# Optimization experiments

Measured on AMD Instinct MI355X. Metric: run time of the kernel, lower is better.

The kernel has to match this reference:

```python
import jax, jax.numpy as jnp
import numpy as np
from jax import lax

BN_EPS = 1e-5
# shifts generated by _generate_shifts(8): dy outer loop, dx inner, skipping (0,0);
# circular_shift rolls shifts=(dx, dy) over dims (2, 3) i.e. dx->H axis, dy->W axis
SHIFTS = [(-1, -1), (0, -1), (1, -1), (-1, 0), (1, 0), (-1, 1), (0, 1), (1, 1)]


def setup_inputs() -> dict:
    key = jax.random.key(0)
    k1, k2 = jax.random.split(key)
    x = jax.random.normal(k1, (32, 128, 56, 56), dtype=jnp.float32)
    # 8 paths, each a 3x3 conv [O, I, kh, kw]
    W = jax.random.normal(k2, (8, 128, 128, 3, 3), dtype=jnp.float32) * 0.05
    gamma = jnp.ones((128,), dtype=jnp.float32)
    beta = jnp.zeros((128,), dtype=jnp.float32)
    return {"x": x, "W": W, "gamma": gamma, "beta": beta}


def _conv3x3(x, w):
    return lax.conv_general_dilated(
        x, w, window_strides=(1, 1), padding=((1, 1), (1, 1)),
        dimension_numbers=("NCHW", "OIHW", "NCHW"))


def reference(x, W, gamma, beta):
    # sum of 8 shifted-input 3x3 convs (accumulated, no stack materialized)
    out = _conv3x3(jnp.roll(x, SHIFTS[0], axis=(2, 3)), W[0])
    for i in range(1, len(SHIFTS)):
        out = out + _conv3x3(jnp.roll(x, SHIFTS[i], axis=(2, 3)), W[i])
    # BatchNorm2d, training-mode batch stats (biased variance), eps=1e-5
    mean = jnp.mean(out, axis=(0, 2, 3), keepdims=True)
    var = jnp.mean(jnp.square(out - mean), axis=(0, 2, 3), keepdims=True)
    out = (out - mean) * lax.rsqrt(var + BN_EPS)
    out = out * gamma.reshape(1, -1, 1, 1) + beta.reshape(1, -1, 1, 1)
    return out
```

## Files before the change

### kernel.cpp

```cpp
#include <hip/hip_runtime.h>
#include <hip/hip_bf16.h>


typedef __attribute__((ext_vector_type(8)))  short s16x8;
typedef __attribute__((ext_vector_type(16))) float f32x16;

__device__ __forceinline__ void gload16(const void* g, void* l) {
    __builtin_amdgcn_global_load_lds(
        (const __attribute__((address_space(1))) unsigned int*)g,
        (__attribute__((address_space(3))) unsigned int*)l, 16, 0, 0);
}

__device__ __forceinline__ unsigned short f2bf(float f) {
    __hip_bfloat16 h = __float2bfloat16(f);
    return *(unsigned short*)&h;
}

__global__ __launch_bounds__(256) void transpose_kernel(
    const float* __restrict__ x, unsigned short* __restrict__ xb,
    float* __restrict__ xcols) {
    __shared__ float xt[128][57];
    const int h = blockIdx.x, n = blockIdx.y, t = threadIdx.x;
    for (int it = 0; it < 28; ++it) {
        int idx = it * 256 + t;
        int c = idx / 56, w = idx % 56;
        xt[c][w] = x[(((size_t)n * 128 + c) * 56 + h) * 56 + w];
    }
    __syncthreads();
    for (int it = 0; it < 4; ++it) {
        int unit = it * 256 + t;
        if (unit < 896) {
            int w = unit >> 4, cu = unit & 15;
            unsigned short pk[8];
#pragma unroll
            for (int j = 0; j < 8; ++j) pk[j] = f2bf(xt[cu * 8 + j][w]);
            *(uint4*)(xb + ((((size_t)n * 56 + h) * 56 + w) * 128 + cu * 8)) = *(uint4*)pk;
        }
    }
    for (int it = 0; it < 2; ++it) {
        int idx = it * 256 + t;
        int c = idx & 127, w4 = idx >> 7;
        const int wmap[4] = {54, 55, 0, 1};
        xcols[(((size_t)n * 4 + w4) * 56 + h) * 128 + c] = xt[c][wmap[w4]];
    }
}

__global__ __launch_bounds__(256) void vpack_kernel(
    const float* __restrict__ W, unsigned short* __restrict__ Ap) {
    int idx = blockIdx.x * 256 + threadIdx.x;
    int tap = idx % 25, oc = idx / 25, c = oc % 128, o = oc / 128;
    int a = tap / 5, b = tap % 5;
    const int dxs[8] = {-1, 0, 1, -1, 1, -1, 0, 1};
    const int dys[8] = {-1, -1, -1, 0, 0, 1, 1, 1};
    float s = 0.f;
#pragma unroll
    for (int i = 0; i < 8; ++i) {
        int kh = a - 1 + dxs[i];
        int kw = b - 1 + dys[i];
        if (kh >= 0 && kh < 3 && kw >= 0 && kw < 3)
            s += W[(((size_t)i * 128 + o) * 128 + c) * 9 + kh * 3 + kw];
    }
    int chunk = c >> 4, k = c & 15, ku = k >> 3, j = k & 7, mo = o >> 5;
    size_t off = ((((size_t)chunk * 25 + tap) * 4 + mo) * 64 + (ku * 32 + (o & 31))) * 8 + j;
    Ap[off] = f2bf(s);
}

__global__ __launch_bounds__(256) void ubuild_kernel(
    const float* __restrict__ W, float* __restrict__ U) {
    int idx = blockIdx.x * 256 + threadIdx.x;
    int c = idx % 128, o = (idx / 128) % 128, e = idx / 16384;
    const int dxs[8] = {-1, 0, 1, -1, 1, -1, 0, 1};
    const int dys[8] = {-1, -1, -1, 0, 0, 1, 1, 1};
    float u[15];
#pragma unroll
    for (int k = 0; k < 15; ++k) u[k] = 0.f;
#pragma unroll
    for (int i = 0; i < 8; ++i) {
        if (e < 2) {
            int kh = (e == 0) ? 0 : 2;
            int hh = (e == 0) ? -1 : 56;
            int sr = (hh - dxs[i] + 56) % 56;
            int r = (e == 0) ? (sr == 54 ? 0 : sr == 55 ? 1 : 2)
                             : (sr == 55 ? 0 : sr == 0 ? 1 : 2);
#pragma unroll
            for (int kw = 0; kw < 3; ++kw) {
                int be = kw - 1 - dys[i] + 2;
                u[r * 5 + be] += W[(((size_t)i * 128 + o) * 128 + c) * 9 + kh * 3 + kw];
            }
        } else {
            int kw = (e == 2) ? 0 : 2;
            int ww = (e == 2) ? -1 : 56;
            int sc = (ww - dys[i] + 56) % 56;
            int r = (e == 2) ? (sc == 54 ? 0 : sc == 55 ? 1 : 2)
                             : (sc == 55 ? 0 : sc == 0 ? 1 : 2);
#pragma unroll
            for (int kh = 0; kh < 3; ++kh) {
                int al = kh - 1 - dxs[i] + 2;
                u[r * 5 + al] += W[(((size_t)i * 128 + o) * 128 + c) * 9 + kh * 3 + kw];
            }
        }
    }
#pragma unroll
    for (int k = 0; k < 15; ++k)
        U[(((size_t)e * 15 + k) * 128 + c) * 128 + o] = u[k];
}

__global__ __launch_bounds__(256) void ucbuild_kernel(
    const float* __restrict__ W, float* __restrict__ Uc) {
    int idx = blockIdx.x * 256 + threadIdx.x;
    int c = idx % 128, o = (idx / 128) % 128, cr = idx / 16384;
    int hC = (cr >> 1) ? 55 : 0, wC = (cr & 1) ? 55 : 0;
    int khb = hC ? 2 : 0, kwb = wC ? 2 : 0;
    const int dxs[8] = {-1, 0, 1, -1, 1, -1, 0, 1};
    const int dys[8] = {-1, -1, -1, 0, 0, 1, 1, 1};
    float v[9];
#pragma unroll
    for (int p = 0; p < 9; ++p) v[p] = 0.f;
#pragma unroll
    for (int i = 0; i < 8; ++i)
        v[(dxs[i] + 1) * 3 + (dys[i] + 1)] = W[(((size_t)i * 128 + o) * 128 + c) * 9 + khb * 3 + kwb];
#pragma unroll
    for (int p = 0; p < 9; ++p)
        Uc[(((size_t)cr * 9 + p) * 128 + c) * 128 + o] = v[p];
}

__global__ __launch_bounds__(512, 2) void conv_mfma(
    const unsigned short* __restrict__ xb, const unsigned short* __restrict__ Ap,
    float* __restrict__ out, float* __restrict__ P) {
    __shared__ __align__(16) unsigned short lds[69632];
    unsigned short* xs = lds;
    unsigned short* As = lds + 16384;
    const int tile = blockIdx.x, n = blockIdx.y;
    const int p0 = tile * 512;
    const int t = threadIdx.x, wv = t >> 6, lane = t & 63;
    const int og = wv >> 2, pg = wv & 3;
    const int hstart = p0 / 56 - 2;

    int vB[4];
    bool fval[4];
#pragma unroll
    for (int nn = 0; nn < 4; ++nn) {
        int px = p0 + pg * 128 + nn * 32 + (lane & 31);
        fval[nn] = px < 3136;
        if (px > 3135) px = 3135;
        int h = px / 56, w = px % 56;
        vB[nn] = (lane >> 5) * 16384 + ((h - hstart - 2) * 60 + w) * 16;
    }
    f32x16 acc[2][4];
#pragma unroll
    for (int mm = 0; mm < 2; ++mm)
#pragma unroll
        for (int nn = 0; nn < 4; ++nn)
#pragma unroll
            for (int r = 0; r < 16; ++r) acc[mm][nn][r] = 0.f;

    const unsigned short* xbn = xb + (size_t)n * 401408;

#pragma unroll 1
    for (int ch = 0; ch < 8; ++ch) {
#pragma unroll
        for (int it = 0; it < 4; ++it) {
            int unit = it * 512 + t;
            int u = unit >> 10, ph = unit & 1023;
            if (ph > 899) ph = 899;
            int r = ph / 60, wc2 = ph % 60;
            int gh = ((hstart + r) % 56 + 56) % 56;
            int gw = wc2 - 2;
            gw += (gw < 0) ? 56 : 0;
            gw -= (gw >= 56) ? 56 : 0;
            gload16(xbn + (gh * 56 + gw) * 128 + ch * 16 + u * 8,
                    (char*)xs + (size_t)(it * 512 + wv * 64) * 16);
        }
        const unsigned short* apc = Ap + (size_t)ch * 51200;
#pragma unroll
        for (int it = 0; it < 13; ++it) {
            int unit = it * 512 + t;
            gload16(apc + (size_t)unit * 8,
                    (char*)As + (size_t)(it * 512 + wv * 64) * 16);
        }
        __syncthreads();

#pragma unroll
        for (int tap = 0; tap < 25; ++tap) {
            const int toff = ((tap / 5) * 60 + (tap % 5)) * 16;
            s16x8 a0 = *(const s16x8*)((const char*)As + (size_t)(tap * 4 + og * 2 + 0) * 1024 + lane * 16);
            s16x8 a1 = *(const s16x8*)((const char*)As + (size_t)(tap * 4 + og * 2 + 1) * 1024 + lane * 16);
            s16x8 b0 = *(const s16x8*)((const char*)xs + vB[0] + toff);
            s16x8 b1 = *(const s16x8*)((const char*)xs + vB[1] + toff);
            s16x8 b2 = *(const s16x8*)((const char*)xs + vB[2] + toff);
            s16x8 b3 = *(const s16x8*)((const char*)xs + vB[3] + toff);
            acc[0][0] = __builtin_amdgcn_mfma_f32_32x32x16_bf16(a0, b0, acc[0][0], 0, 0, 0);
            acc[1][0] = __builtin_amdgcn_mfma_f32_32x32x16_bf16(a1, b0, acc[1][0], 0, 0, 0);
            acc[0][1] = __builtin_amdgcn_mfma_f32_32x32x16_bf16(a0, b1, acc[0][1], 0, 0, 0);
            acc[1][1] = __builtin_amdgcn_mfma_f32_32x32x16_bf16(a1, b1, acc[1][1], 0, 0, 0);
            acc[0][2] = __builtin_amdgcn_mfma_f32_32x32x16_bf16(a0, b2, acc[0][2], 0, 0, 0);
            acc[1][2] = __builtin_amdgcn_mfma_f32_32x32x16_bf16(a1, b2, acc[1][2], 0, 0, 0);
            acc[0][3] = __builtin_amdgcn_mfma_f32_32x32x16_bf16(a0, b3, acc[0][3], 0, 0, 0);
            acc[1][3] = __builtin_amdgcn_mfma_f32_32x32x16_bf16(a1, b3, acc[1][3], 0, 0, 0);
        }
        __syncthreads();
    }

    const int slot = (n * 7 + tile) * 4 + pg;
#pragma unroll
    for (int mm = 0; mm < 2; ++mm) {
#pragma unroll
        for (int r = 0; r < 16; ++r) {
            int o = og * 64 + mm * 32 + (r & 3) + ((lane >> 5) << 2) + ((r >> 2) << 3);
            float s = 0.f, q = 0.f;
#pragma unroll
            for (int nn = 0; nn < 4; ++nn) {
                if (fval[nn]) {
                    float v = acc[mm][nn][r];
                    size_t oi = ((size_t)(n * 128 + o)) * 3136 + (p0 + pg * 128 + nn * 32 + (lane & 31));
                    out[oi] = v;
                    s += v;
                    q = fmaf(v, v, q);
                }
            }
#pragma unroll
            for (int off = 1; off < 32; off <<= 1) {
                s += __shfl_xor(s, off);
                q += __shfl_xor(q, off);
            }
            if ((lane & 31) == 0) {
                P[((size_t)slot * 2 + 0) * 128 + o] = s;
                P[((size_t)slot * 2 + 1) * 128 + o] = q;
            }
        }
    }
}

__global__ __launch_bounds__(512) void border_kernel(
    const float* __restrict__ x, const float* __restrict__ xcols,
    const float* __restrict__ U,
    float* __restrict__ corrRow, float* __restrict__ corrCol) {
    __shared__ float xsb[3][128][33];
    __shared__ float red[2][2][64][15];
    const int e = blockIdx.x, n = blockIdx.y, part = blockIdx.z;
    const int t = threadIdx.x, lane = t & 63, wv = t >> 6;
    const int oh = wv & 1, qh = (wv >> 1) & 1, chalf = wv >> 2;
    int rows[3];
    if (e == 0 || e == 2) { rows[0] = 54; rows[1] = 55; rows[2] = 0; }
    else                  { rows[0] = 55; rows[1] = 0;  rows[2] = 1; }
    if (e < 2) {
        for (int it = 0; it < 24; ++it) {
            int idx = it * 512 + t;
            int m = idx & 31, c = (idx >> 5) & 127, r = idx >> 12;
            int g = part * 28 + m - 2;
            g += (g < 0) ? 56 : 0;
            g -= (g >= 56) ? 56 : 0;
            xsb[r][c][m] = x[(((size_t)n * 128 + c) * 56 + rows[r]) * 56 + g];
        }
    } else {
        int w4[3];
#pragma unroll
        for (int r = 0; r < 3; ++r)
            w4[r] = (rows[r] == 54) ? 0 : (rows[r] == 55) ? 1 : (rows[r] == 0) ? 2 : 3;
        for (int it = 0; it < 24; ++it) {
            int idx = it * 512 + t;
            int c = idx & 127, m = (idx >> 7) & 31, r = idx >> 12;
            int g = part * 28 + m - 2;
            g += (g < 0) ? 56 : 0;
            g -= (g >= 56) ? 56 : 0;
            xsb[r][c][m] = xcols[(((size_t)n * 4 + w4[r]) * 56 + g) * 128 + c];
        }
    }
    __syncthreads();
    const int o = oh * 64 + lane;
    const int pxl = qh * 14;
    float corr[14];
#pragma unroll
    for (int k = 0; k < 14; ++k) corr[k] = 0.f;
#pragma unroll 2
    for (int ci = 0; ci < 64; ++ci) {
        const int c = chalf * 64 + ci;
#pragma unroll
        for (int r = 0; r < 3; ++r) {
            float xl[18];
#pragma unroll
            for (int j = 0; j < 18; ++j) xl[j] = xsb[r][c][pxl + j];
#pragma unroll
            for (int be = 0; be < 5; ++be) {
                float u = U[(((size_t)e * 15 + r * 5 + be) * 128 + c) * 128 + o];
#pragma unroll
                for (int k = 0; k < 14; ++k) corr[k] = fmaf(u, xl[k + be], corr[k]);
            }
        }
    }
    if (chalf == 1) {
#pragma unroll
        for (int k = 0; k < 14; ++k) red[qh][oh][lane][k] = corr[k];
    }
    __syncthreads();
    if (chalf == 0) {
#pragma unroll
        for (int k = 0; k < 14; ++k) corr[k] += red[qh][oh][lane][k];
        const int pbase = part * 28 + qh * 14;
        float* dst = (e < 2 ? corrRow + (((size_t)e * 32 + n) * 128 + o) * 56
                            : corrCol + (((size_t)(e - 2) * 32 + n) * 128 + o) * 56) + pbase;
#pragma unroll
        for (int k = 0; k < 14; ++k) dst[k] = corr[k];
    }
}

__global__ __launch_bounds__(256) void corner_kernel(
    const float* __restrict__ xcols, const float* __restrict__ Uc,
    float* __restrict__ cadd) {
    __shared__ float xc[9][128];
    __shared__ float red[2][128];
    const int cr = blockIdx.x, n = blockIdx.y, t = threadIdx.x;
    const int hC = (cr >> 1) ? 55 : 0, wC = (cr & 1) ? 55 : 0;
    const int khb = hC ? 2 : 0, kwb = wC ? 2 : 0;
    for (int it = 0; it < 5; ++it) {
        int idx = it * 256 + t;
        if (idx < 1152) {
            int c = idx & 127, p = idx >> 7;
            int di = p / 3, dj = p % 3;
            int hs = (hC + khb - 1 - (di - 1) + 56) % 56;
            int ws = (wC + kwb - 1 - (dj - 1) + 56) % 56;
            int w4 = (ws == 54) ? 0 : (ws == 55) ? 1 : (ws == 0) ? 2 : 3;
            xc[p][c] = xcols[(((size_t)n * 4 + w4) * 56 + hs) * 128 + c];
        }
    }
    __syncthreads();
    const int o = t & 127, half = t >> 7;
    float corr = 0.f;
    const float* ucb = Uc + ((size_t)cr * 9 * 128) * 128 + o;
#pragma unroll 4
    for (int pc = half * 576; pc < half * 576 + 576; ++pc) {
        int p = pc >> 7, c = pc & 127;
        corr = fmaf(ucb[(size_t)pc * 128], xc[p][c], corr);
    }
    red[half][o] = corr;
    __syncthreads();
    if (t < 128)
        cadd[(size_t)cr * 4096 + n * 128 + t] = red[0][t] + red[1][t];
}

__global__ __launch_bounds__(256) void finalize_kernel(
    const float* __restrict__ P, const float* __restrict__ out,
    const float* __restrict__ corrRow, const float* __restrict__ corrCol,
    const float* __restrict__ cadd,
    const float* __restrict__ gamma, const float* __restrict__ beta,
    float* __restrict__ SS) {
    const int c = blockIdx.x, t = threadIdx.x;
    float s = 0.f, q = 0.f;
    for (int sl = t; sl < 896; sl += 256) {
        s += P[((size_t)sl * 2 + 0) * 128 + c];
        q += P[((size_t)sl * 2 + 1) * 128 + c];
    }
    for (int item = t; item < 7040; item += 256) {
        int n = item / 220, bidx = item % 220;
        int h, w;
        if (bidx < 56)       { h = 0;  w = bidx; }
        else if (bidx < 112) { h = 55; w = bidx - 56; }
        else if (bidx < 166) { w = 0;  h = bidx - 111; }
        else                 { w = 55; h = bidx - 165; }
        float d = 0.f;
        if (h == 0)  d -= corrRow[(((size_t)0 * 32 + n) * 128 + c) * 56 + w];
        if (h == 55) d -= corrRow[(((size_t)1 * 32 + n) * 128 + c) * 56 + w];
        if (w == 0)  d -= corrCol[(((size_t)0 * 32 + n) * 128 + c) * 56 + h];
        if (w == 55) d -= corrCol[(((size_t)1 * 32 + n) * 128 + c) * 56 + h];
        if ((h == 0 || h == 55) && (w == 0 || w == 55)) {
            int cr = (h ? 2 : 0) + (w ? 1 : 0);
            d += cadd[(size_t)cr * 4096 + n * 128 + c];
        }
        float old = out[((size_t)(n * 128 + c)) * 3136 + h * 56 + w];
        s += d;
        q += d * d + 2.f * old * d;
    }
    __shared__ float rs[256], rq[256];
    rs[t] = s; rq[t] = q;
    __syncthreads();
    for (int st = 128; st > 0; st >>= 1) {
        if (t < st) { rs[t] += rs[t + st]; rq[t] += rq[t + st]; }
        __syncthreads();
    }
    if (t == 0) {
        const float inv = 1.f / 100352.f;
        float mean = rs[0] * inv;
        float var  = rq[0] * inv - mean * mean;
        float sc = gamma[c] * rsqrtf(var + 1e-5f);
        SS[c] = sc;
        SS[128 + c] = beta[c] - mean * sc;
    }
}

__global__ __launch_bounds__(256) void bn_apply_kernel(
    float* __restrict__ out, const float* __restrict__ SS,
    const float* __restrict__ corrRow, const float* __restrict__ corrCol,
    const float* __restrict__ cadd) {
    size_t idx = (size_t)blockIdx.x * 256 + threadIdx.x;
    int plane = (int)(idx / 784);
    int rem = (int)(idx % 784);
    int h = rem / 14, w4 = (rem % 14) * 4;
    int c = plane & 127, n = plane >> 7;
    float sc = SS[c], sh = SS[128 + c];
    float4 v = ((float4*)out)[idx];
    float d0 = 0.f, d1 = 0.f, d2 = 0.f, d3 = 0.f;
    if (h == 0 || h == 55) {
        int eh = (h == 55) ? 1 : 0;
        const float4 cr4 = *(const float4*)(corrRow + (((size_t)eh * 32 + n) * 128 + c) * 56 + w4);
        d0 -= cr4.x; d1 -= cr4.y; d2 -= cr4.z; d3 -= cr4.w;
    }
    if (w4 == 0)  d0 -= corrCol[(((size_t)0 * 32 + n) * 128 + c) * 56 + h];
    if (w4 == 52) d3 -= corrCol[(((size_t)1 * 32 + n) * 128 + c) * 56 + h];
    if (h == 0 || h == 55) {
        int hb = (h == 55) ? 2 : 0;
        if (w4 == 0)  d0 += cadd[(size_t)(hb + 0) * 4096 + n * 128 + c];
        if (w4 == 52) d3 += cadd[(size_t)(hb + 1) * 4096 + n * 128 + c];
    }
    v.x = fmaf(v.x + d0, sc, sh);
    v.y = fmaf(v.y + d1, sc, sh);
    v.z = fmaf(v.z + d2, sc, sh);
    v.w = fmaf(v.w + d3, sc, sh);
    ((float4*)out)[idx] = v;
}

extern "C" void kernel_launch(void* const* d_in, const int* in_sizes, int n_in,
                              void* d_out, int out_size, void* d_ws, size_t ws_size,
                              hipStream_t stream) {
    const float* x     = (const float*)d_in[0];
    const float* W     = (const float*)d_in[1];
    const float* gamma = (const float*)d_in[2];
    const float* beta  = (const float*)d_in[3];
    float* out = (float*)d_out;

    char* ws = (char*)d_ws;
    unsigned short* xb = (unsigned short*)ws;
    unsigned short* Ap = (unsigned short*)(ws + 25690112);
    float* U       = (float*)(ws + 26513408);
    float* Uc      = (float*)(ws + 30445568);
    float* P       = (float*)(ws + 32804864);
    float* SS      = (float*)(ws + 34017280);
    float* xcols   = (float*)(ws + 34018304);
    float* corrRow = (float*)(ws + 37688320);
    float* corrCol = (float*)(ws + 39523328);
    float* cadd    = (float*)(ws + 41358336);

    transpose_kernel<<<dim3(56, 32), 256, 0, stream>>>(x, xb, xcols);
    vpack_kernel<<<1600, 256, 0, stream>>>(W, Ap);
    ubuild_kernel<<<256, 256, 0, stream>>>(W, U);
    ucbuild_kernel<<<256, 256, 0, stream>>>(W, Uc);
    conv_mfma<<<dim3(7, 32), 512, 0, stream>>>(xb, Ap, out, P);
    border_kernel<<<dim3(4, 32, 2), 512, 0, stream>>>(x, xcols, U, corrRow, corrCol);
    corner_kernel<<<dim3(4, 32), 256, 0, stream>>>(xcols, Uc, cadd);
    finalize_kernel<<<128, 256, 0, stream>>>(P, out, corrRow, corrCol, cadd, gamma, beta, SS);
    bn_apply_kernel<<<12544, 256, 0, stream>>>(out, SS, corrRow, corrCol, cadd);
}
```

Before: 324.1 us.

## Restructure conv MFMA kernel into 4-wave blocks with double-buffered LDS pipeline

The conv kernel now runs 256 threads per block, with each wave computing all 128 output channels for its pixel group (a 4x4 accumulator tile) instead of splitting channels across two wave groups. Input and weight tiles are double-buffered in LDS and prefetched with explicit vmcnt waits and raw barriers, so the next tap-row's weights and the next channel chunk's input load while MFMAs run. This aims to hide global-load latency and raise MFMA reuse per LDS read. The cost is a doubled accumulator register footprint and fewer waves per CU. The circular-wrap modulo is also replaced with conditional adds.

```diff
diff --git a/kernel.cpp b/kernel.cpp
--- a/kernel.cpp
+++ b/kernel.cpp
@@ -124,16 +124,14 @@
         Uc[(((size_t)cr * 9 + p) * 128 + c) * 128 + o] = v[p];
 }
 
-__global__ __launch_bounds__(512, 2) void conv_mfma(
+__global__ __launch_bounds__(256, 1) void conv_mfma(
     const unsigned short* __restrict__ xb, const unsigned short* __restrict__ Ap,
     float* __restrict__ out, float* __restrict__ P) {
-    __shared__ __align__(16) unsigned short lds[69632];
-    unsigned short* xs = lds;
-    unsigned short* As = lds + 16384;
+    __shared__ __align__(16) unsigned short lds[53248];
     const int tile = blockIdx.x, n = blockIdx.y;
     const int p0 = tile * 512;
     const int t = threadIdx.x, wv = t >> 6, lane = t & 63;
-    const int og = wv >> 2, pg = wv & 3;
+    const int pg = wv;
     const int hstart = p0 / 56 - 2;
 
     int vB[4];
@@ -146,9 +144,9 @@
         int h = px / 56, w = px % 56;
         vB[nn] = (lane >> 5) * 16384 + ((h - hstart - 2) * 60 + w) * 16;
     }
-    f32x16 acc[2][4];
-#pragma unroll
-    for (int mm = 0; mm < 2; ++mm)
+    f32x16 acc[4][4];
+#pragma unroll
+    for (int mm = 0; mm < 4; ++mm)
 #pragma unroll
         for (int nn = 0; nn < 4; ++nn)
 #pragma unroll
@@ -156,57 +154,100 @@
 
     const unsigned short* xbn = xb + (size_t)n * 401408;
 
-#pragma unroll 1
-    for (int ch = 0; ch < 8; ++ch) {
-#pragma unroll
-        for (int it = 0; it < 4; ++it) {
-            int unit = it * 512 + t;
+    auto stage_xs = [&](int ch, int buf) {
+#pragma unroll
+        for (int it = 0; it < 8; ++it) {
+            int unit = it * 256 + t;
             int u = unit >> 10, ph = unit & 1023;
             if (ph > 899) ph = 899;
             int r = ph / 60, wc2 = ph % 60;
-            int gh = ((hstart + r) % 56 + 56) % 56;
+            int gh = hstart + r;
+            gh += (gh < 0) ? 56 : 0;
+            gh -= (gh >= 56) ? 56 : 0;
             int gw = wc2 - 2;
             gw += (gw < 0) ? 56 : 0;
             gw -= (gw >= 56) ? 56 : 0;
             gload16(xbn + (gh * 56 + gw) * 128 + ch * 16 + u * 8,
-                    (char*)xs + (size_t)(it * 512 + wv * 64) * 16);
-        }
-        const unsigned short* apc = Ap + (size_t)ch * 51200;
-#pragma unroll
-        for (int it = 0; it < 13; ++it) {
-            int unit = it * 512 + t;
-            gload16(apc + (size_t)unit * 8,
-                    (char*)As + (size_t)(it * 512 + wv * 64) * 16);
-        }
-        __syncthreads();
-
-#pragma unroll
-        for (int tap = 0; tap < 25; ++tap) {
-            const int toff = ((tap / 5) * 60 + (tap % 5)) * 16;
-            s16x8 a0 = *(const s16x8*)((const char*)As + (size_t)(tap * 4 + og * 2 + 0) * 1024 + lane * 16);
-            s16x8 a1 = *(const s16x8*)((const char*)As + (size_t)(tap * 4 + og * 2 + 1) * 1024 + lane * 16);
-            s16x8 b0 = *(const s16x8*)((const char*)xs + vB[0] + toff);
-            s16x8 b1 = *(const s16x8*)((const char*)xs + vB[1] + toff);
-            s16x8 b2 = *(const s16x8*)((const char*)xs + vB[2] + toff);
-            s16x8 b3 = *(const s16x8*)((const char*)xs + vB[3] + toff);
-            acc[0][0] = __builtin_amdgcn_mfma_f32_32x32x16_bf16(a0, b0, acc[0][0], 0, 0, 0);
-            acc[1][0] = __builtin_amdgcn_mfma_f32_32x32x16_bf16(a1, b0, acc[1][0], 0, 0, 0);
-            acc[0][1] = __builtin_amdgcn_mfma_f32_32x32x16_bf16(a0, b1, acc[0][1], 0, 0, 0);
-            acc[1][1] = __builtin_amdgcn_mfma_f32_32x32x16_bf16(a1, b1, acc[1][1], 0, 0, 0);
-            acc[0][2] = __builtin_amdgcn_mfma_f32_32x32x16_bf16(a0, b2, acc[0][2], 0, 0, 0);
-            acc[1][2] = __builtin_amdgcn_mfma_f32_32x32x16_bf16(a1, b2, acc[1][2], 0, 0, 0);
-            acc[0][3] = __builtin_amdgcn_mfma_f32_32x32x16_bf16(a0, b3, acc[0][3], 0, 0, 0);
-            acc[1][3] = __builtin_amdgcn_mfma_f32_32x32x16_bf16(a1, b3, acc[1][3], 0, 0, 0);
-        }
-        __syncthreads();
+                    (char*)lds + buf * 32768 + (size_t)(it * 256 + wv * 64) * 16);
+        }
+    };
+    auto stage_A = [&](int ch, int tg, int buf) {
+        const unsigned short* src = Ap + (size_t)ch * 51200 + tg * 10240;
+#pragma unroll
+        for (int it = 0; it < 5; ++it) {
+            int unit = it * 256 + t;
+            gload16(src + (size_t)unit * 8,
+                    (char*)lds + 65536 + buf * 20480 + (size_t)(it * 256 + wv * 64) * 16);
+        }
+    };
+
+    stage_xs(0, 0);
+    stage_A(0, 0, 0);
+    asm volatile("s_waitcnt vmcnt(0)" ::: "memory");
+    __builtin_amdgcn_s_barrier();
+    asm volatile("" ::: "memory");
+
+    int abuf = 0;
+#pragma unroll 1
+    for (int ch = 0; ch < 8; ++ch) {
+#pragma unroll 1
+        for (int tg = 0; tg < 5; ++tg) {
+            const bool last = (ch == 7 && tg == 4);
+            if (!last) {
+                int nch = (tg == 4) ? ch + 1 : ch;
+                int ntg = (tg == 4) ? 0 : tg + 1;
+                stage_A(nch, ntg, abuf ^ 1);
+            }
+            bool xsIss = false;
+            if (tg == 0 && ch < 7) { stage_xs(ch + 1, (ch + 1) & 1); xsIss = true; }
+            if (last)       asm volatile("s_waitcnt vmcnt(0)"  ::: "memory");
+            else if (xsIss) asm volatile("s_waitcnt vmcnt(13)" ::: "memory");
+            else            asm volatile("s_waitcnt vmcnt(5)"  ::: "memory");
+            __builtin_amdgcn_s_barrier();
+            asm volatile("" ::: "memory");
+
+            const char* xsBase = (const char*)lds + (ch & 1) * 32768;
+            const char* aBase  = (const char*)lds + 65536 + abuf * 20480;
+            const int rowoff = tg * 960;
+#pragma unroll
+            for (int tl = 0; tl < 5; ++tl) {
+                const int toff = rowoff + tl * 16;
+                s16x8 a0 = *(const s16x8*)(aBase + (size_t)(tl * 4 + 0) * 1024 + lane * 16);
+                s16x8 a1 = *(const s16x8*)(aBase + (size_t)(tl * 4 + 1) * 1024 + lane * 16);
+                s16x8 a2 = *(const s16x8*)(aBase + (size_t)(tl * 4 + 2) * 1024 + lane * 16);
+                s16x8 a3 = *(const s16x8*)(aBase + (size_t)(tl * 4 + 3) * 1024 + lane * 16);
+                s16x8 b0 = *(const s16x8*)(xsBase + vB[0] + toff);
+                s16x8 b1 = *(const s16x8*)(xsBase + vB[1] + toff);
+                s16x8 b2 = *(const s16x8*)(xsBase + vB[2] + toff);
+                s16x8 b3 = *(const s16x8*)(xsBase + vB[3] + toff);
+                acc[0][0] = __builtin_amdgcn_mfma_f32_32x32x16_bf16(a0, b0, acc[0][0], 0, 0, 0);
+                acc[0][1] = __builtin_amdgcn_mfma_f32_32x32x16_bf16(a0, b1, acc[0][1], 0, 0, 0);
+                acc[0][2] = __builtin_amdgcn_mfma_f32_32x32x16_bf16(a0, b2, acc[0][2], 0, 0, 0);
+                acc[0][3] = __builtin_amdgcn_mfma_f32_32x32x16_bf16(a0, b3, acc[0][3], 0, 0, 0);
+                acc[1][0] = __builtin_amdgcn_mfma_f32_32x32x16_bf16(a1, b0, acc[1][0], 0, 0, 0);
+                acc[1][1] = __builtin_amdgcn_mfma_f32_32x32x16_bf16(a1, b1, acc[1][1], 0, 0, 0);
+                acc[1][2] = __builtin_amdgcn_mfma_f32_32x32x16_bf16(a1, b2, acc[1][2], 0, 0, 0);
+                acc[1][3] = __builtin_amdgcn_mfma_f32_32x32x16_bf16(a1, b3, acc[1][3], 0, 0, 0);
+                acc[2][0] = __builtin_amdgcn_mfma_f32_32x32x16_bf16(a2, b0, acc[2][0], 0, 0, 0);
+                acc[2][1] = __builtin_amdgcn_mfma_f32_32x32x16_bf16(a2, b1, acc[2][1], 0, 0, 0);
+                acc[2][2] = __builtin_amdgcn_mfma_f32_32x32x16_bf16(a2, b2, acc[2][2], 0, 0, 0);
+                acc[2][3] = __builtin_amdgcn_mfma_f32_32x32x16_bf16(a2, b3, acc[2][3], 0, 0, 0);
+                acc[3][0] = __builtin_amdgcn_mfma_f32_32x32x16_bf16(a3, b0, acc[3][0], 0, 0, 0);
+                acc[3][1] = __builtin_amdgcn_mfma_f32_32x32x16_bf16(a3, b1, acc[3][1], 0, 0, 0);
+                acc[3][2] = __builtin_amdgcn_mfma_f32_32x32x16_bf16(a3, b2, acc[3][2], 0, 0, 0);
+                acc[3][3] = __builtin_amdgcn_mfma_f32_32x32x16_bf16(a3, b3, acc[3][3], 0, 0, 0);
+            }
+            __builtin_amdgcn_s_barrier();
+            abuf ^= 1;
+        }
     }
 
     const int slot = (n * 7 + tile) * 4 + pg;
 #pragma unroll
-    for (int mm = 0; mm < 2; ++mm) {
+    for (int mm = 0; mm < 4; ++mm) {
 #pragma unroll
         for (int r = 0; r < 16; ++r) {
-            int o = og * 64 + mm * 32 + (r & 3) + ((lane >> 5) << 2) + ((r >> 2) << 3);
+            int o = mm * 32 + (r & 3) + ((lane >> 5) << 2) + ((r >> 2) << 3);
             float s = 0.f, q = 0.f;
 #pragma unroll
             for (int nn = 0; nn < 4; ++nn) {
@@ -443,7 +484,7 @@
     vpack_kernel<<<1600, 256, 0, stream>>>(W, Ap);
     ubuild_kernel<<<256, 256, 0, stream>>>(W, U);
     ucbuild_kernel<<<256, 256, 0, stream>>>(W, Uc);
-    conv_mfma<<<dim3(7, 32), 512, 0, stream>>>(xb, Ap, out, P);
+    conv_mfma<<<dim3(7, 32), 256, 0, stream>>>(xb, Ap, out, P);
     border_kernel<<<dim3(4, 32, 2), 512, 0, stream>>>(x, xcols, U, corrRow, corrCol);
     corner_kernel<<<dim3(4, 32), 256, 0, stream>>>(xcols, Uc, cadd);
     finalize_kernel<<<128, 256, 0, stream>>>(P, out, corrRow, corrCol, cadd, gamma, beta, SS);
```

After: 336.3 us. +3.8%, slower.

## Double-buffer conv input tiles, read weights from global, merge weight-prep kernels

Applied to the files above, without the earlier changes.

The conv kernel now double-buffers the input halo tile in LDS, so the next channel chunk is prefetched while the current one is computed. The weight fragments are read straight from global memory (through the caches) instead of being staged in LDS, which shrinks LDS use and changes launch bounds to one block per CU. The three weight-preparation kernels are merged into a single launch to cut launch overhead, and the row wrap uses conditional adds instead of a modulo. The risks are higher latency on the per-tap global weight loads and less latency hiding at the lower occupancy.

```diff
diff --git a/kernel.cpp b/kernel.cpp
--- a/kernel.cpp
+++ b/kernel.cpp
@@ -45,91 +45,83 @@
     }
 }
 
-__global__ __launch_bounds__(256) void vpack_kernel(
-    const float* __restrict__ W, unsigned short* __restrict__ Ap) {
-    int idx = blockIdx.x * 256 + threadIdx.x;
-    int tap = idx % 25, oc = idx / 25, c = oc % 128, o = oc / 128;
-    int a = tap / 5, b = tap % 5;
+__global__ __launch_bounds__(256) void wprep_kernel(
+    const float* __restrict__ W, unsigned short* __restrict__ Ap,
+    float* __restrict__ U, float* __restrict__ Uc) {
+    const int bx = blockIdx.x, t = threadIdx.x;
     const int dxs[8] = {-1, 0, 1, -1, 1, -1, 0, 1};
     const int dys[8] = {-1, -1, -1, 0, 0, 1, 1, 1};
-    float s = 0.f;
-#pragma unroll
-    for (int i = 0; i < 8; ++i) {
-        int kh = a - 1 + dxs[i];
-        int kw = b - 1 + dys[i];
-        if (kh >= 0 && kh < 3 && kw >= 0 && kw < 3)
-            s += W[(((size_t)i * 128 + o) * 128 + c) * 9 + kh * 3 + kw];
-    }
-    int chunk = c >> 4, k = c & 15, ku = k >> 3, j = k & 7, mo = o >> 5;
-    size_t off = ((((size_t)chunk * 25 + tap) * 4 + mo) * 64 + (ku * 32 + (o & 31))) * 8 + j;
-    Ap[off] = f2bf(s);
-}
-
-__global__ __launch_bounds__(256) void ubuild_kernel(
-    const float* __restrict__ W, float* __restrict__ U) {
-    int idx = blockIdx.x * 256 + threadIdx.x;
-    int c = idx % 128, o = (idx / 128) % 128, e = idx / 16384;
-    const int dxs[8] = {-1, 0, 1, -1, 1, -1, 0, 1};
-    const int dys[8] = {-1, -1, -1, 0, 0, 1, 1, 1};
-    float u[15];
-#pragma unroll
-    for (int k = 0; k < 15; ++k) u[k] = 0.f;
-#pragma unroll
-    for (int i = 0; i < 8; ++i) {
-        if (e < 2) {
-            int kh = (e == 0) ? 0 : 2;
-            int hh = (e == 0) ? -1 : 56;
-            int sr = (hh - dxs[i] + 56) % 56;
-            int r = (e == 0) ? (sr == 54 ? 0 : sr == 55 ? 1 : 2)
-                             : (sr == 55 ? 0 : sr == 0 ? 1 : 2);
-#pragma unroll
-            for (int kw = 0; kw < 3; ++kw) {
-                int be = kw - 1 - dys[i] + 2;
-                u[r * 5 + be] += W[(((size_t)i * 128 + o) * 128 + c) * 9 + kh * 3 + kw];
+    if (bx < 1600) {
+        int idx = bx * 256 + t;
+        int tap = idx % 25, oc = idx / 25, c = oc % 128, o = oc / 128;
+        int a = tap / 5, b = tap % 5;
+        float s = 0.f;
+#pragma unroll
+        for (int i = 0; i < 8; ++i) {
+            int kh = a - 1 + dxs[i];
+            int kw = b - 1 + dys[i];
+            if (kh >= 0 && kh < 3 && kw >= 0 && kw < 3)
+                s += W[(((size_t)i * 128 + o) * 128 + c) * 9 + kh * 3 + kw];
+        }
+        int chunk = c >> 4, k = c & 15, ku = k >> 3, j = k & 7, mo = o >> 5;
+        size_t off = ((((size_t)chunk * 25 + tap) * 4 + mo) * 64 + (ku * 32 + (o & 31))) * 8 + j;
+        Ap[off] = f2bf(s);
+    } else if (bx < 1856) {
+        int idx = (bx - 1600) * 256 + t;
+        int c = idx % 128, o = (idx / 128) % 128, e = idx / 16384;
+        float u[15];
+#pragma unroll
+        for (int k = 0; k < 15; ++k) u[k] = 0.f;
+#pragma unroll
+        for (int i = 0; i < 8; ++i) {
+            if (e < 2) {
+                int kh = (e == 0) ? 0 : 2;
+                int hh = (e == 0) ? -1 : 56;
+                int sr = (hh - dxs[i] + 56) % 56;
+                int r = (e == 0) ? (sr == 54 ? 0 : sr == 55 ? 1 : 2)
+                                 : (sr == 55 ? 0 : sr == 0 ? 1 : 2);
+#pragma unroll
+                for (int kw = 0; kw < 3; ++kw) {
+                    int be = kw - 1 - dys[i] + 2;
+                    u[r * 5 + be] += W[(((size_t)i * 128 + o) * 128 + c) * 9 + kh * 3 + kw];
+                }
+            } else {
+                int kw = (e == 2) ? 0 : 2;
+                int ww = (e == 2) ? -1 : 56;
+                int sc = (ww - dys[i] + 56) % 56;
+                int r = (e == 2) ? (sc == 54 ? 0 : sc == 55 ? 1 : 2)
+                                 : (sc == 55 ? 0 : sc == 0 ? 1 : 2);
+#pragma unroll
+                for (int kh = 0; kh < 3; ++kh) {
+                    int al = kh - 1 - dxs[i] + 2;
+                    u[r * 5 + al] += W[(((size_t)i * 128 + o) * 128 + c) * 9 + kh * 3 + kw];
+                }
             }
-        } else {
-            int kw = (e == 2) ? 0 : 2;
-            int ww = (e == 2) ? -1 : 56;
-            int sc = (ww - dys[i] + 56) % 56;
-            int r = (e == 2) ? (sc == 54 ? 0 : sc == 55 ? 1 : 2)
-                             : (sc == 55 ? 0 : sc == 0 ? 1 : 2);
-#pragma unroll
-            for (int kh = 0; kh < 3; ++kh) {
-                int al = kh - 1 - dxs[i] + 2;
-                u[r * 5 + al] += W[(((size_t)i * 128 + o) * 128 + c) * 9 + kh * 3 + kw];
-            }
-        }
-    }
-#pragma unroll
-    for (int k = 0; k < 15; ++k)
-        U[(((size_t)e * 15 + k) * 128 + c) * 128 + o] = u[k];
-}
-
-__global__ __launch_bounds__(256) void ucbuild_kernel(
-    const float* __restrict__ W, float* __restrict__ Uc) {
-    int idx = blockIdx.x * 256 + threadIdx.x;
-    int c = idx % 128, o = (idx / 128) % 128, cr = idx / 16384;
-    int hC = (cr >> 1) ? 55 : 0, wC = (cr & 1) ? 55 : 0;
-    int khb = hC ? 2 : 0, kwb = wC ? 2 : 0;
-    const int dxs[8] = {-1, 0, 1, -1, 1, -1, 0, 1};
-    const int dys[8] = {-1, -1, -1, 0, 0, 1, 1, 1};
-    float v[9];
-#pragma unroll
-    for (int p = 0; p < 9; ++p) v[p] = 0.f;
-#pragma unroll
-    for (int i = 0; i < 8; ++i)
-        v[(dxs[i] + 1) * 3 + (dys[i] + 1)] = W[(((size_t)i * 128 + o) * 128 + c) * 9 + khb * 3 + kwb];
-#pragma unroll
-    for (int p = 0; p < 9; ++p)
-        Uc[(((size_t)cr * 9 + p) * 128 + c) * 128 + o] = v[p];
-}
-
-__global__ __launch_bounds__(512, 2) void conv_mfma(
+        }
+#pragma unroll
+        for (int k = 0; k < 15; ++k)
+            U[(((size_t)e * 15 + k) * 128 + c) * 128 + o] = u[k];
+    } else {
+        int idx = (bx - 1856) * 256 + t;
+        int c = idx % 128, o = (idx / 128) % 128, cr = idx / 16384;
+        int hC = (cr >> 1) ? 55 : 0, wC = (cr & 1) ? 55 : 0;
+        int khb = hC ? 2 : 0, kwb = wC ? 2 : 0;
+        float v[9];
+#pragma unroll
+        for (int p = 0; p < 9; ++p) v[p] = 0.f;
+#pragma unroll
+        for (int i = 0; i < 8; ++i)
+            v[(dxs[i] + 1) * 3 + (dys[i] + 1)] = W[(((size_t)i * 128 + o) * 128 + c) * 9 + khb * 3 + kwb];
+#pragma unroll
+        for (int p = 0; p < 9; ++p)
+            Uc[(((size_t)cr * 9 + p) * 128 + c) * 128 + o] = v[p];
+    }
+}
+
+__global__ __launch_bounds__(512, 1) void conv_mfma(
     const unsigned short* __restrict__ xb, const unsigned short* __restrict__ Ap,
     float* __restrict__ out, float* __restrict__ P) {
-    __shared__ __align__(16) unsigned short lds[69632];
-    unsigned short* xs = lds;
-    unsigned short* As = lds + 16384;
+    __shared__ __align__(16) unsigned short lds[32768];
     const int tile = blockIdx.x, n = blockIdx.y;
     const int p0 = tile * 512;
     const int t = threadIdx.x, wv = t >> 6, lane = t & 63;
@@ -155,40 +147,43 @@
             for (int r = 0; r < 16; ++r) acc[mm][nn][r] = 0.f;
 
     const unsigned short* xbn = xb + (size_t)n * 401408;
-
-#pragma unroll 1
-    for (int ch = 0; ch < 8; ++ch) {
+    const unsigned short* apw = Ap + (size_t)(og * 2) * 512 + lane * 8;
+
+    auto stage_xs = [&](int ch, int buf) {
 #pragma unroll
         for (int it = 0; it < 4; ++it) {
             int unit = it * 512 + t;
             int u = unit >> 10, ph = unit & 1023;
             if (ph > 899) ph = 899;
             int r = ph / 60, wc2 = ph % 60;
-            int gh = ((hstart + r) % 56 + 56) % 56;
+            int gh = hstart + r;
+            gh += (gh < 0) ? 56 : 0;
+            gh -= (gh >= 56) ? 56 : 0;
             int gw = wc2 - 2;
             gw += (gw < 0) ? 56 : 0;
             gw -= (gw >= 56) ? 56 : 0;
             gload16(xbn + (gh * 56 + gw) * 128 + ch * 16 + u * 8,
-                    (char*)xs + (size_t)(it * 512 + wv * 64) * 16);
-        }
-        const unsigned short* apc = Ap + (size_t)ch * 51200;
-#pragma unroll
-        for (int it = 0; it < 13; ++it) {
-            int unit = it * 512 + t;
-            gload16(apc + (size_t)unit * 8,
-                    (char*)As + (size_t)(it * 512 + wv * 64) * 16);
-        }
-        __syncthreads();
-
+                    (char*)lds + buf * 32768 + (size_t)(it * 512 + wv * 64) * 16);
+        }
+    };
+
+    stage_xs(0, 0);
+    __syncthreads();
+
+#pragma unroll 1
+    for (int ch = 0; ch < 8; ++ch) {
+        if (ch < 7) stage_xs(ch + 1, (ch + 1) & 1);
+        const char* xsBase = (const char*)lds + (ch & 1) * 32768;
+        const unsigned short* apc = apw + (size_t)ch * 51200;
 #pragma unroll
         for (int tap = 0; tap < 25; ++tap) {
             const int toff = ((tap / 5) * 60 + (tap % 5)) * 16;
-            s16x8 a0 = *(const s16x8*)((const char*)As + (size_t)(tap * 4 + og * 2 + 0) * 1024 + lane * 16);
-            s16x8 a1 = *(const s16x8*)((const char*)As + (size_t)(tap * 4 + og * 2 + 1) * 1024 + lane * 16);
-            s16x8 b0 = *(const s16x8*)((const char*)xs + vB[0] + toff);
-            s16x8 b1 = *(const s16x8*)((const char*)xs + vB[1] + toff);
-            s16x8 b2 = *(const s16x8*)((const char*)xs + vB[2] + toff);
-            s16x8 b3 = *(const s16x8*)((const char*)xs + vB[3] + toff);
+            s16x8 a0 = *(const s16x8*)(apc + (size_t)tap * 2048);
+            s16x8 a1 = *(const s16x8*)(apc + (size_t)tap * 2048 + 512);
+            s16x8 b0 = *(const s16x8*)(xsBase + vB[0] + toff);
+            s16x8 b1 = *(const s16x8*)(xsBase + vB[1] + toff);
+            s16x8 b2 = *(const s16x8*)(xsBase + vB[2] + toff);
+            s16x8 b3 = *(const s16x8*)(xsBase + vB[3] + toff);
             acc[0][0] = __builtin_amdgcn_mfma_f32_32x32x16_bf16(a0, b0, acc[0][0], 0, 0, 0);
             acc[1][0] = __builtin_amdgcn_mfma_f32_32x32x16_bf16(a1, b0, acc[1][0], 0, 0, 0);
             acc[0][1] = __builtin_amdgcn_mfma_f32_32x32x16_bf16(a0, b1, acc[0][1], 0, 0, 0);
@@ -440,9 +435,7 @@
     float* cadd    = (float*)(ws + 41358336);
 
     transpose_kernel<<<dim3(56, 32), 256, 0, stream>>>(x, xb, xcols);
-    vpack_kernel<<<1600, 256, 0, stream>>>(W, Ap);
-    ubuild_kernel<<<256, 256, 0, stream>>>(W, U);
-    ucbuild_kernel<<<256, 256, 0, stream>>>(W, Uc);
+    wprep_kernel<<<2112, 256, 0, stream>>>(W, Ap, U, Uc);
     conv_mfma<<<dim3(7, 32), 512, 0, stream>>>(xb, Ap, out, P);
     border_kernel<<<dim3(4, 32, 2), 512, 0, stream>>>(x, xcols, U, corrRow, corrCol);
     corner_kernel<<<dim3(4, 32), 256, 0, stream>>>(xcols, Uc, cadd);
```

After: 315.9 us. 2.5% less time.
